# Optimization experiments

Hardware: AMD Instinct MI355X
Metric: run time of the kernel (lower is better)

The kernel has to match this reference:

```python
import jax, jax.numpy as jnp
import numpy as np

N = 512
D = 400          # per-sample feature dim (lstm_hidden_dim * 2)
H = 400          # hidden dim of F_func (lstm_hidden_dim * 2)


def setup_inputs() -> dict:
    key = jax.random.key(0)
    k1, k2, k3, k4, k5, k6 = jax.random.split(key, 6)
    x_samples = jax.random.normal(k1, (N, D), dtype=jnp.float32)
    y_samples = jax.random.normal(k2, (N, D), dtype=jnp.float32)
    # torch nn.Linear default init: U(-1/sqrt(fan_in), 1/sqrt(fan_in))
    b1_bound = 1.0 / np.sqrt(2 * D)
    b2_bound = 1.0 / np.sqrt(H)
    W1 = jax.random.uniform(k3, (H, 2 * D), minval=-b1_bound, maxval=b1_bound, dtype=jnp.float32)
    b1 = jax.random.uniform(k4, (H,), minval=-b1_bound, maxval=b1_bound, dtype=jnp.float32)
    W2 = jax.random.uniform(k5, (1, H), minval=-b2_bound, maxval=b2_bound, dtype=jnp.float32)
    b2 = jax.random.uniform(k6, (1,), minval=-b2_bound, maxval=b2_bound, dtype=jnp.float32)
    return {"x_samples": x_samples, "y_samples": y_samples,
            "W1": W1, "b1": b1, "W2": W2, "b2": b2}


def reference(x_samples, y_samples, W1, b1, W2, b2):
    n = y_samples.shape[0]
    W1x, W1y = W1[:, :D], W1[:, D:]
    hx = x_samples @ W1x.T          # [N, H], contribution of x
    hy = y_samples @ W1y.T          # [N, H], contribution of y

    def score(h):  # second linear + softplus, squeeze out last dim of 1
        return jax.nn.softplus(h @ W2.T + b2)[..., 0]

    # T0[i] = F(x[i], y[i])
    T0 = score(jax.nn.relu(hx + hy + b1))                      # [N]
    # T1[i, j] = F(x[j], y[i])  (x tiled along dim 0, y along dim 1)
    h_pair = jax.nn.relu(hy[:, None, :] + hx[None, :, :] + b1) # [N, N, H]
    T1 = score(h_pair)                                          # [N, N]

    t0_mean = T0.mean()
    lower_bound = t0_mean - (jax.nn.logsumexp(T1, axis=1).mean() - jnp.log(jnp.float32(n)))
    upper_bound = t0_mean - T1.mean()
    return (lower_bound, upper_bound)
```

## Files before the change

### kernel.cpp

```cpp
#include <hip/hip_runtime.h>
#include <math.h>


#define NSAMP 512
#define DIM 400
#define HID 400

__global__ __launch_bounds__(256) void club_gemm_kernel(
    const float* __restrict__ X, const float* __restrict__ Y,
    const float* __restrict__ W1, const float* __restrict__ b1,
    float* __restrict__ hxT, float* __restrict__ hyb)
{
    __shared__ __align__(16) float Ls[64 * 204];
    const int t    = threadIdx.x;
    const int lane = t & 63;
    const int wave = __builtin_amdgcn_readfirstlane(t >> 6);
    const int b    = blockIdx.x;

    const float* __restrict__ Lbase;
    const float* __restrict__ Sbase;
    int Lstride, Lcol0, Lrow0, Lrowmax;
    int Sstride, Scol0, Srow0, Srowmax;
    float* __restrict__ D;
    int Dstride, Dcol0;
    int mat;

    if (b < 104) {
        mat = 0;
        const int bx = b & 7, by = b >> 3;
        Lbase = X;  Lstride = DIM;     Lcol0 = 0;   Lrow0 = bx * 64; Lrowmax = NSAMP - 1;
        Sbase = W1; Sstride = 2 * DIM; Scol0 = 0;   Srow0 = by * 32; Srowmax = HID - 1;
        D = hxT; Dstride = NSAMP; Dcol0 = bx * 64;
    } else {
        mat = 1;
        const int bb = b - 104;
        const int bx = bb & 15, by = bb >> 4;
        Lbase = W1; Lstride = 2 * DIM; Lcol0 = DIM; Lrow0 = by * 64; Lrowmax = HID - 1;
        Sbase = Y;  Sstride = DIM;     Scol0 = 0;   Srow0 = bx * 32; Srowmax = NSAMP - 1;
        D = hyb; Dstride = HID; Dcol0 = by * 64;
    }

    float acc[8];
#pragma unroll
    for (int c = 0; c < 8; c++) acc[c] = 0.f;

    const int srow_base = Srow0 + wave * 8;

    for (int kc = 0; kc < DIM; kc += 200) {
        __syncthreads();
        for (int idx = t; idx < 3200; idx += 256) {
            int row = idx / 50, q = idx % 50;
            int r = Lrow0 + row; if (r > Lrowmax) r = Lrowmax;
            float4 v = *(const float4*)(Lbase + (size_t)r * Lstride + Lcol0 + kc + 4 * q);
            *(float4*)(Ls + row * 204 + 4 * q) = v;
        }
        __syncthreads();
#pragma unroll 2
        for (int k4 = 0; k4 < 50; k4++) {
            float4 xv = *(const float4*)(Ls + lane * 204 + 4 * k4);
#pragma unroll
            for (int c = 0; c < 8; c++) {
                int sr = srow_base + c; if (sr > Srowmax) sr = Srowmax;
                float4 wv = *(const float4*)(Sbase + (size_t)sr * Sstride + Scol0 + kc + 4 * k4);
                acc[c] = fmaf(xv.x, wv.x, acc[c]);
                acc[c] = fmaf(xv.y, wv.y, acc[c]);
                acc[c] = fmaf(xv.z, wv.z, acc[c]);
                acc[c] = fmaf(xv.w, wv.w, acc[c]);
            }
        }
    }

    if (mat == 1) {
        int hl = Lrow0 + lane; if (hl > HID - 1) hl = HID - 1;
        float bv = b1[hl];
#pragma unroll
        for (int c = 0; c < 8; c++) acc[c] += bv;
        if (Lrow0 + lane < HID) {
#pragma unroll
            for (int c = 0; c < 8; c++) {
                int sr = srow_base + c;
                D[(size_t)sr * Dstride + Dcol0 + lane] = acc[c];
            }
        }
    } else {
#pragma unroll
        for (int c = 0; c < 8; c++) {
            int sr = srow_base + c;
            if (sr < HID)
                D[(size_t)sr * Dstride + Dcol0 + lane] = acc[c];
        }
    }
}

__global__ __launch_bounds__(256) void club_pair_kernel(
    const float* __restrict__ hxT, const float* __restrict__ hyb,
    const float* __restrict__ W2, const float* __restrict__ b2,
    double* __restrict__ expsum, double* __restrict__ tsum,
    double* __restrict__ diagT)
{
    const int t    = threadIdx.x;
    const int lane = t & 63;
    const int wave = __builtin_amdgcn_readfirstlane(t >> 6);
    const int j0   = blockIdx.x * 64;
    const int j    = j0 + lane;
    const int i0   = blockIdx.y * 16 + wave * 4;

    float acc[4] = {0.f, 0.f, 0.f, 0.f};

    const float* __restrict__ Bp = hxT + j;

#pragma unroll 2
    for (int g = 0; g < 50; g++) {
        const int h = 8 * g;
        float bv[8];
#pragma unroll
        for (int u = 0; u < 8; u++)
            bv[u] = Bp[(size_t)(h + u) * NSAMP];
        const float* __restrict__ wp = W2 + h;
#pragma unroll
        for (int r = 0; r < 4; r++) {
            const float* __restrict__ ap = hyb + (size_t)(i0 + r) * HID + h;
            float a;
#pragma unroll
            for (int u = 0; u < 8; u++) {
                a = ap[u] + bv[u];
                acc[r] = fmaf(fmaxf(a, 0.f), wp[u], acc[r]);
            }
        }
    }

    const float bb2 = b2[0];
#pragma unroll
    for (int r = 0; r < 4; r++) {
        const int i = i0 + r;
        float s  = acc[r] + bb2;
        float es = expf(s);
        float T  = log1pf(es);
        if (j == i) diagT[i] = (double)T;
        double eD = 1.0 + (double)es;
        double tD = (double)T;
        for (int off = 32; off > 0; off >>= 1) {
            eD += __shfl_down(eD, off);
            tD += __shfl_down(tD, off);
        }
        if (lane == 0) {
            expsum[i * 8 + blockIdx.x] = eD;
            tsum  [i * 8 + blockIdx.x] = tD;
        }
    }
}

__global__ __launch_bounds__(512) void club_final_kernel(
    const double* __restrict__ expsum, const double* __restrict__ tsum,
    const double* __restrict__ diagT, float* __restrict__ out)
{
    __shared__ double sh[3 * 512];
    const int t = threadIdx.x;
    double es = 0.0, ts = 0.0;
#pragma unroll
    for (int b = 0; b < 8; b++) { es += expsum[t * 8 + b]; ts += tsum[t * 8 + b]; }
    sh[t] = log(es); sh[512 + t] = ts; sh[1024 + t] = diagT[t];
    __syncthreads();
    for (int off = 256; off > 0; off >>= 1) {
        if (t < off) {
            sh[t]        += sh[t + off];
            sh[512 + t]  += sh[512 + t + off];
            sh[1024 + t] += sh[1024 + t + off];
        }
        __syncthreads();
    }
    if (t == 0) {
        double t0m  = sh[1024] / 512.0;
        double lsem = sh[0]    / 512.0;
        double t1m  = sh[512]  / (512.0 * 512.0);
        out[0] = (float)(t0m - (lsem - log(512.0)));
        out[1] = (float)(t0m - t1m);
    }
}

extern "C" void kernel_launch(void* const* d_in, const int* in_sizes, int n_in,
                              void* d_out, int out_size, void* d_ws, size_t ws_size,
                              hipStream_t stream) {
    const float* X  = (const float*)d_in[0];
    const float* Y  = (const float*)d_in[1];
    const float* W1 = (const float*)d_in[2];
    const float* b1 = (const float*)d_in[3];
    const float* W2 = (const float*)d_in[4];
    const float* b2 = (const float*)d_in[5];
    float* out = (float*)d_out;

    char* ws = (char*)d_ws;
    float*  hxT    = (float*) (ws);
    float*  hyb    = (float*) (ws +  819200);
    double* expsum = (double*)(ws + 1638400);
    double* tsum   = (double*)(ws + 1671168);
    double* diagT  = (double*)(ws + 1703936);

    club_gemm_kernel <<<dim3(216),    256, 0, stream>>>(X, Y, W1, b1, hxT, hyb);
    club_pair_kernel <<<dim3(8, 32),  256, 0, stream>>>(hxT, hyb, W2, b2,
                                                        expsum, tsum, diagT);
    club_final_kernel<<<1, 512, 0, stream>>>(expsum, tsum, diagT, out);
}
```

Before: 136.1 us.

## Split GEMM over K halves with combine pass and finer pair-kernel grid

The projection GEMM is split into two K halves, each written to its own partial buffer, and uses 4 rows per wave instead of 8, which raises the block count from 216 to 848. A new combine kernel sums the partial buffers. The pair kernel now handles one i row per wave with two interleaved accumulators and vectorized hyb/W2 loads, over a 4x larger grid. The goal is better occupancy across CUs, at the cost of an extra launch and extra global memory traffic for the partial buffers.

```diff
diff --git a/kernel.cpp b/kernel.cpp
--- a/kernel.cpp
+++ b/kernel.cpp
@@ -9,7 +9,8 @@
 __global__ __launch_bounds__(256) void club_gemm_kernel(
     const float* __restrict__ X, const float* __restrict__ Y,
     const float* __restrict__ W1, const float* __restrict__ b1,
-    float* __restrict__ hxT, float* __restrict__ hyb)
+    float* __restrict__ hxT0, float* __restrict__ hxT1,
+    float* __restrict__ hyb0, float* __restrict__ hyb1)
 {
     __shared__ __align__(16) float Ls[64 * 204];
     const int t    = threadIdx.x;
@@ -19,76 +20,83 @@
 
     const float* __restrict__ Lbase;
     const float* __restrict__ Sbase;
-    int Lstride, Lcol0, Lrow0, Lrowmax;
-    int Sstride, Scol0, Srow0, Srowmax;
-    float* __restrict__ D;
-    int Dstride, Dcol0;
-    int mat;
-
-    if (b < 104) {
-        mat = 0;
-        const int bx = b & 7, by = b >> 3;
+    int Lstride, Lcol0, Lrow0, Lrowmax, Sstride, Scol0, srow_base;
+    int kh, mat;
+
+    if (b < 400) {
+        mat = 0; kh = b & 1;
+        const int bx = (b >> 1) & 7, by = b >> 4;
         Lbase = X;  Lstride = DIM;     Lcol0 = 0;   Lrow0 = bx * 64; Lrowmax = NSAMP - 1;
-        Sbase = W1; Sstride = 2 * DIM; Scol0 = 0;   Srow0 = by * 32; Srowmax = HID - 1;
-        D = hxT; Dstride = NSAMP; Dcol0 = bx * 64;
+        Sbase = W1; Sstride = 2 * DIM; Scol0 = 0;
+        srow_base = by * 16 + wave * 4;
     } else {
         mat = 1;
-        const int bb = b - 104;
-        const int bx = bb & 15, by = bb >> 4;
+        const int bb = b - 400; kh = bb & 1;
+        const int bx = (bb >> 1) & 31, by = bb >> 6;
         Lbase = W1; Lstride = 2 * DIM; Lcol0 = DIM; Lrow0 = by * 64; Lrowmax = HID - 1;
-        Sbase = Y;  Sstride = DIM;     Scol0 = 0;   Srow0 = bx * 32; Srowmax = NSAMP - 1;
-        D = hyb; Dstride = HID; Dcol0 = by * 64;
-    }
-
-    float acc[8];
-#pragma unroll
-    for (int c = 0; c < 8; c++) acc[c] = 0.f;
-
-    const int srow_base = Srow0 + wave * 8;
-
-    for (int kc = 0; kc < DIM; kc += 200) {
-        __syncthreads();
-        for (int idx = t; idx < 3200; idx += 256) {
-            int row = idx / 50, q = idx % 50;
-            int r = Lrow0 + row; if (r > Lrowmax) r = Lrowmax;
-            float4 v = *(const float4*)(Lbase + (size_t)r * Lstride + Lcol0 + kc + 4 * q);
-            *(float4*)(Ls + row * 204 + 4 * q) = v;
+        Sbase = Y;  Sstride = DIM;     Scol0 = 0;
+        srow_base = bx * 16 + wave * 4;
+    }
+    const int kc0 = kh * 200;
+
+    for (int idx = t; idx < 3200; idx += 256) {
+        int row = idx / 50, q = idx % 50;
+        int r = Lrow0 + row; if (r > Lrowmax) r = Lrowmax;
+        float4 v = *(const float4*)(Lbase + (size_t)r * Lstride + Lcol0 + kc0 + 4 * q);
+        *(float4*)(Ls + row * 204 + 4 * q) = v;
+    }
+    __syncthreads();
+
+    float acc[4] = {0.f, 0.f, 0.f, 0.f};
+#pragma unroll 2
+    for (int k4 = 0; k4 < 50; k4++) {
+        float4 xv = *(const float4*)(Ls + lane * 204 + 4 * k4);
+#pragma unroll
+        for (int c = 0; c < 4; c++) {
+            const float* __restrict__ wp =
+                Sbase + (size_t)(srow_base + c) * Sstride + Scol0 + kc0 + 4 * k4;
+            float4 wv = *(const float4*)wp;
+            acc[c] = fmaf(xv.x, wv.x, acc[c]);
+            acc[c] = fmaf(xv.y, wv.y, acc[c]);
+            acc[c] = fmaf(xv.z, wv.z, acc[c]);
+            acc[c] = fmaf(xv.w, wv.w, acc[c]);
         }
-        __syncthreads();
-#pragma unroll 2
-        for (int k4 = 0; k4 < 50; k4++) {
-            float4 xv = *(const float4*)(Ls + lane * 204 + 4 * k4);
-#pragma unroll
-            for (int c = 0; c < 8; c++) {
-                int sr = srow_base + c; if (sr > Srowmax) sr = Srowmax;
-                float4 wv = *(const float4*)(Sbase + (size_t)sr * Sstride + Scol0 + kc + 4 * k4);
-                acc[c] = fmaf(xv.x, wv.x, acc[c]);
-                acc[c] = fmaf(xv.y, wv.y, acc[c]);
-                acc[c] = fmaf(xv.z, wv.z, acc[c]);
-                acc[c] = fmaf(xv.w, wv.w, acc[c]);
+    }
+
+    if (mat == 0) {
+        float* __restrict__ dst = kh ? hxT1 : hxT0;
+#pragma unroll
+        for (int c = 0; c < 4; c++)
+            dst[(size_t)(srow_base + c) * NSAMP + Lrow0 + lane] = acc[c];
+    } else {
+        float* __restrict__ dst = kh ? hyb1 : hyb0;
+        const int h = Lrow0 + lane;
+        if (h < HID) {
+            if (kh == 0) {
+                float bv = b1[h];
+#pragma unroll
+                for (int c = 0; c < 4; c++) acc[c] += bv;
             }
+#pragma unroll
+            for (int c = 0; c < 4; c++)
+                dst[(size_t)(srow_base + c) * HID + h] = acc[c];
         }
     }
-
-    if (mat == 1) {
-        int hl = Lrow0 + lane; if (hl > HID - 1) hl = HID - 1;
-        float bv = b1[hl];
-#pragma unroll
-        for (int c = 0; c < 8; c++) acc[c] += bv;
-        if (Lrow0 + lane < HID) {
-#pragma unroll
-            for (int c = 0; c < 8; c++) {
-                int sr = srow_base + c;
-                D[(size_t)sr * Dstride + Dcol0 + lane] = acc[c];
-            }
-        }
+}
+
+__global__ __launch_bounds__(256) void club_combine_kernel(
+    const float4* __restrict__ hxT0, const float4* __restrict__ hxT1,
+    const float4* __restrict__ hyb0, const float4* __restrict__ hyb1,
+    float4* __restrict__ hxT, float4* __restrict__ hyb)
+{
+    const int idx = blockIdx.x * 256 + threadIdx.x;
+    if (idx < 51200) {
+        float4 a = hxT0[idx], b = hxT1[idx];
+        hxT[idx] = make_float4(a.x + b.x, a.y + b.y, a.z + b.z, a.w + b.w);
     } else {
-#pragma unroll
-        for (int c = 0; c < 8; c++) {
-            int sr = srow_base + c;
-            if (sr < HID)
-                D[(size_t)sr * Dstride + Dcol0 + lane] = acc[c];
-        }
+        const int k = idx - 51200;
+        float4 a = hyb0[k], b = hyb1[k];
+        hyb[k] = make_float4(a.x + b.x, a.y + b.y, a.z + b.z, a.w + b.w);
     }
 }
 
@@ -101,14 +109,14 @@
     const int t    = threadIdx.x;
     const int lane = t & 63;
     const int wave = __builtin_amdgcn_readfirstlane(t >> 6);
-    const int j0   = blockIdx.x * 64;
-    const int j    = j0 + lane;
-    const int i0   = blockIdx.y * 16 + wave * 4;
-
-    float acc[4] = {0.f, 0.f, 0.f, 0.f};
+    const int jx   = blockIdx.x;
+    const int j    = jx * 64 + lane;
+    const int i    = blockIdx.y * 4 + wave;
 
     const float* __restrict__ Bp = hxT + j;
-
+    const float* __restrict__ Ap = hyb + (size_t)i * HID;
+
+    float acc0 = 0.f, acc1 = 0.f;
 #pragma unroll 2
     for (int g = 0; g < 50; g++) {
         const int h = 8 * g;
@@ -116,37 +124,33 @@
 #pragma unroll
         for (int u = 0; u < 8; u++)
             bv[u] = Bp[(size_t)(h + u) * NSAMP];
-        const float* __restrict__ wp = W2 + h;
-#pragma unroll
-        for (int r = 0; r < 4; r++) {
-            const float* __restrict__ ap = hyb + (size_t)(i0 + r) * HID + h;
-            float a;
-#pragma unroll
-            for (int u = 0; u < 8; u++) {
-                a = ap[u] + bv[u];
-                acc[r] = fmaf(fmaxf(a, 0.f), wp[u], acc[r]);
-            }
-        }
-    }
-
-    const float bb2 = b2[0];
-#pragma unroll
-    for (int r = 0; r < 4; r++) {
-        const int i = i0 + r;
-        float s  = acc[r] + bb2;
-        float es = expf(s);
-        float T  = log1pf(es);
-        if (j == i) diagT[i] = (double)T;
-        double eD = 1.0 + (double)es;
-        double tD = (double)T;
-        for (int off = 32; off > 0; off >>= 1) {
-            eD += __shfl_down(eD, off);
-            tD += __shfl_down(tD, off);
-        }
-        if (lane == 0) {
-            expsum[i * 8 + blockIdx.x] = eD;
-            tsum  [i * 8 + blockIdx.x] = tD;
-        }
+        float4 a0 = *(const float4*)(Ap + h);
+        float4 a1 = *(const float4*)(Ap + h + 4);
+        float4 w0 = *(const float4*)(W2 + h);
+        float4 w1 = *(const float4*)(W2 + h + 4);
+        acc0 = fmaf(fmaxf(a0.x + bv[0], 0.f), w0.x, acc0);
+        acc1 = fmaf(fmaxf(a0.y + bv[1], 0.f), w0.y, acc1);
+        acc0 = fmaf(fmaxf(a0.z + bv[2], 0.f), w0.z, acc0);
+        acc1 = fmaf(fmaxf(a0.w + bv[3], 0.f), w0.w, acc1);
+        acc0 = fmaf(fmaxf(a1.x + bv[4], 0.f), w1.x, acc0);
+        acc1 = fmaf(fmaxf(a1.y + bv[5], 0.f), w1.y, acc1);
+        acc0 = fmaf(fmaxf(a1.z + bv[6], 0.f), w1.z, acc0);
+        acc1 = fmaf(fmaxf(a1.w + bv[7], 0.f), w1.w, acc1);
+    }
+
+    float s  = (acc0 + acc1) + b2[0];
+    float es = expf(s);
+    float T  = log1pf(es);
+    if (j == i) diagT[i] = (double)T;
+    double eD = 1.0 + (double)es;
+    double tD = (double)T;
+    for (int off = 32; off > 0; off >>= 1) {
+        eD += __shfl_down(eD, off);
+        tD += __shfl_down(tD, off);
+    }
+    if (lane == 0) {
+        expsum[i * 8 + jx] = eD;
+        tsum  [i * 8 + jx] = tD;
     }
 }
 
@@ -190,14 +194,22 @@
     float* out = (float*)d_out;
 
     char* ws = (char*)d_ws;
-    float*  hxT    = (float*) (ws);
-    float*  hyb    = (float*) (ws +  819200);
-    double* expsum = (double*)(ws + 1638400);
-    double* tsum   = (double*)(ws + 1671168);
-    double* diagT  = (double*)(ws + 1703936);
-
-    club_gemm_kernel <<<dim3(216),    256, 0, stream>>>(X, Y, W1, b1, hxT, hyb);
-    club_pair_kernel <<<dim3(8, 32),  256, 0, stream>>>(hxT, hyb, W2, b2,
-                                                        expsum, tsum, diagT);
-    club_final_kernel<<<1, 512, 0, stream>>>(expsum, tsum, diagT, out);
-}
+    float*  hxT0   = (float*) (ws);
+    float*  hxT1   = (float*) (ws +  819200);
+    float*  hyb0   = (float*) (ws + 1638400);
+    float*  hyb1   = (float*) (ws + 2457600);
+    float*  hxT    = (float*) (ws + 3276800);
+    float*  hyb    = (float*) (ws + 4096000);
+    double* expsum = (double*)(ws + 4915200);
+    double* tsum   = (double*)(ws + 4947968);
+    double* diagT  = (double*)(ws + 4980736);
+
+    club_gemm_kernel   <<<dim3(848),    256, 0, stream>>>(X, Y, W1, b1,
+                                                          hxT0, hxT1, hyb0, hyb1);
+    club_combine_kernel<<<dim3(400),    256, 0, stream>>>((const float4*)hxT0, (const float4*)hxT1,
+                                                          (const float4*)hyb0, (const float4*)hyb1,
+                                                          (float4*)hxT, (float4*)hyb);
+    club_pair_kernel   <<<dim3(8, 128), 256, 0, stream>>>(hxT, hyb, W2, b2,
+                                                          expsum, tsum, diagT);
+    club_final_kernel  <<<1, 512, 0, stream>>>(expsum, tsum, diagT, out);
+}
```

Result: faster. 110.1 us (-19.1%).
